# Performance work log

Measured on AMD Instinct MI355X. Metric: run time of the kernel, lower is better.

Reference implementation:

```python
import jax, jax.numpy as jnp
import numpy as np
from jax import lax

R, D, K = 8192, 1024, 1203          # proposals, feat dim, foreground classes
M = 128                             # per-class pre-NMS candidate budget (static)
TOPK = 300                          # test_topk_per_image
SCORE_THRESH = 1e-4
NMS_THRESH = 0.5
IMG_H, IMG_W = 800.0, 1333.0
NEG = -1e9
SCALE_CLAMP = float(np.log(1000.0 / 16.0))
BBOX_W = (10.0, 10.0, 5.0, 5.0)     # Box2BoxTransform weights


def setup_inputs() -> dict:
    key = jax.random.key(0)
    k0, k1, k2, k3 = jax.random.split(key, 4)
    feat = jax.random.normal(k0, (R, D), jnp.float32)
    u = jax.random.uniform(k1, (R, 4), jnp.float32)
    x1 = u[:, 0] * 1000.0
    y1 = u[:, 1] * 600.0
    bw = u[:, 2] * 300.0 + 16.0
    bh = u[:, 3] * 300.0 + 16.0
    proposals = jnp.stack([x1, y1, x1 + bw, y1 + bh], axis=1)  # [R,4] xyxy
    w_cls = jax.random.normal(k2, (D, K + 1), jnp.float32) * 0.02
    b_cls = jnp.zeros((K + 1,), jnp.float32)
    w_box = jax.random.normal(k3, (D, 4), jnp.float32) * 0.01
    b_box = jnp.zeros((4,), jnp.float32)
    return dict(feat=feat, proposals=proposals, w_cls=w_cls, b_cls=b_cls,
                w_box=w_box, b_box=b_box)


def _apply_deltas(deltas, boxes):
    # detectron2 Box2BoxTransform.apply_deltas, class-agnostic (R,4)
    wx, wy, ww, wh = BBOX_W
    widths = boxes[:, 2] - boxes[:, 0]
    heights = boxes[:, 3] - boxes[:, 1]
    ctr_x = boxes[:, 0] + 0.5 * widths
    ctr_y = boxes[:, 1] + 0.5 * heights
    dx = deltas[:, 0] / wx
    dy = deltas[:, 1] / wy
    dw = jnp.minimum(deltas[:, 2] / ww, SCALE_CLAMP)
    dh = jnp.minimum(deltas[:, 3] / wh, SCALE_CLAMP)
    pcx = dx * widths + ctr_x
    pcy = dy * heights + ctr_y
    pw = jnp.exp(dw) * widths
    ph = jnp.exp(dh) * heights
    return jnp.stack([pcx - 0.5 * pw, pcy - 0.5 * ph,
                      pcx + 0.5 * pw, pcy + 0.5 * ph], axis=1)


def _clip_boxes(b):
    x1 = jnp.clip(b[:, 0], 0.0, IMG_W)
    y1 = jnp.clip(b[:, 1], 0.0, IMG_H)
    x2 = jnp.clip(b[:, 2], 0.0, IMG_W)
    y2 = jnp.clip(b[:, 3], 0.0, IMG_H)
    return jnp.stack([x1, y1, x2, y2], axis=1)


def _iou_matrix(b):  # [M,4] -> [M,M]
    area = (b[:, 2] - b[:, 0]) * (b[:, 3] - b[:, 1])
    lt = jnp.maximum(b[:, None, :2], b[None, :, :2])
    rb = jnp.minimum(b[:, None, 2:], b[None, :, 2:])
    wh = jnp.clip(rb - lt, 0.0)
    inter = wh[..., 0] * wh[..., 1]
    return inter / (area[:, None] + area[None, :] - inter + 1e-6)


def _forward(feat, proposals, w_cls, b_cls, w_box, b_box):
    # dense heads
    logits = feat @ w_cls + b_cls                      # [R, K+1]
    probs = jax.nn.softmax(logits, axis=-1)
    scores = probs[:, :-1]                             # drop background -> [R, K]
    deltas = feat @ w_box + b_box                      # [R, 4] (class-agnostic)
    boxes = _clip_boxes(_apply_deltas(deltas, proposals))  # [R, 4]

    # score-threshold filter (masking instead of nonzero, jit-safe)
    masked = jnp.where(scores > SCORE_THRESH, scores, NEG)  # [R, K]

    def nms_one_class(cls_scores):  # [R] -> kept scores [M], proposal ids [M]
        vals, idx = lax.top_k(cls_scores, M)
        valid = vals > NEG * 0.5
        b = boxes[idx]                                 # [M, 4]
        iou = _iou_matrix(b)                           # [M, M]

        def body(keep, i):
            suppressed = jnp.any(keep & (iou[:, i] > NMS_THRESH))
            ki = valid[i] & jnp.logical_not(suppressed)
            return keep.at[i].set(ki), None

        keep, _ = lax.scan(body, jnp.zeros((M,), bool), jnp.arange(M))
        return jnp.where(keep, vals, NEG), idx

    per_scores, per_idx = jax.vmap(nms_one_class)(masked.T)  # [K, M] each

    # global top-k over surviving detections
    flat_scores = per_scores.reshape(-1)               # [K*M]
    top_vals, top_i = lax.top_k(flat_scores, TOPK)
    cls_ids = top_i // M                               # pred class per detection
    prop_ids = per_idx.reshape(-1)[top_i]              # original proposal index
    out_boxes = boxes[prop_ids]                        # [TOPK, 4]
    # pack: [x1,y1,x2,y2,score,class]
    return jnp.concatenate(
        [out_boxes, top_vals[:, None], cls_ids.astype(jnp.float32)[:, None]],
        axis=1)


def reference(feat, proposals, w_cls, b_cls, w_box, b_box):
    return _forward(feat, proposals, w_cls, b_cls, w_box, b_box)
```

## Files before the change

kernel.cpp:

```cpp
#include <hip/hip_runtime.h>
#include <math.h>
#include <stdint.h>

#define RR 8192
#define DD 1024
#define KCLS 1203
#define KP 1204
#define KP2 1216
#define NB 1280
#define MM 128
#define TOPKN 300
#define NFLAT (KCLS * MM)
#define NEGV (-1e9f)
#define SCLAMP 4.1351665567423563f

typedef __attribute__((ext_vector_type(8))) short bf16x8;
typedef __attribute__((ext_vector_type(4))) float f32x4;

__device__ __forceinline__ unsigned fmono(float f) {
  unsigned u = __float_as_uint(f);
  return (u & 0x80000000u) ? ~u : (u | 0x80000000u);
}
__device__ __forceinline__ float monof(unsigned u) {
  return __uint_as_float((u & 0x80000000u) ? (u ^ 0x80000000u) : ~u);
}
__device__ __forceinline__ float iou_f(float4 a, float4 b) {
  float areaA = (a.z - a.x) * (a.w - a.y);
  float areaB = (b.z - b.x) * (b.w - b.y);
  float lx = fmaxf(a.x, b.x), ly = fmaxf(a.y, b.y);
  float rx = fminf(a.z, b.z), ry = fminf(a.w, b.w);
  float w = fmaxf(rx - lx, 0.f), h = fmaxf(ry - ly, 0.f);
  float inter = w * h;
  return inter / (areaA + areaB - inter + 1e-6f);
}

__device__ __forceinline__ unsigned short bf16_rn(float x) {
  unsigned u = __float_as_uint(x);
  unsigned r = (u + 0x7FFFu + ((u >> 16) & 1u)) >> 16;
  return (unsigned short)r;
}
__device__ __forceinline__ float bf16f(unsigned short h) {
  return __uint_as_float(((unsigned)h) << 16);
}
__device__ __forceinline__ void split3(float x, unsigned short& h, unsigned short& m2, unsigned short& l) {
  h = bf16_rn(x);
  float r1 = x - bf16f(h);
  m2 = bf16_rn(r1);
  float r2 = r1 - bf16f(m2);
  l = bf16_rn(r2);
}

__global__ __launch_bounds__(256) void k_split_feat(const float* __restrict__ feat,
                                                    unsigned short* __restrict__ Ap) {
  const size_t i4 = (size_t)blockIdx.x * 256 + threadIdx.x;
  float4 v = *(const float4*)&feat[i4 * 4];
  ushort4 h, m2, l;
  split3(v.x, h.x, m2.x, l.x);
  split3(v.y, h.y, m2.y, l.y);
  split3(v.z, h.z, m2.z, l.z);
  split3(v.w, h.w, m2.w, l.w);
  const size_t P = (size_t)RR * DD;
  *(ushort4*)&Ap[0 * P + i4 * 4] = h;
  *(ushort4*)&Ap[1 * P + i4 * 4] = m2;
  *(ushort4*)&Ap[2 * P + i4 * 4] = l;
}

__global__ __launch_bounds__(256) void k_split_w(const float* __restrict__ wcls,
                                                 unsigned short* __restrict__ Btp) {
  __shared__ float st[64][65];
  const int c0 = blockIdx.x * 64, k0 = blockIdx.y * 64;
  const int tid = threadIdx.x;
  const int cc = tid & 63, kq = tid >> 6;
  for (int it = 0; it < 16; ++it) {
    int kl = it * 4 + kq;
    int c = c0 + cc;
    st[cc][kl] = (c < KP) ? wcls[(size_t)(k0 + kl) * KP + c] : 0.f;
  }
  __syncthreads();
  const int kk = tid & 63, cq = tid >> 6;
  const size_t P = (size_t)NB * DD;
  for (int it = 0; it < 16; ++it) {
    int cl = it * 4 + cq;
    float v = st[cl][kk];
    unsigned short h, m2, l;
    split3(v, h, m2, l);
    size_t off = (size_t)(c0 + cl) * DD + k0 + kk;
    Btp[0 * P + off] = h;
    Btp[1 * P + off] = m2;
    Btp[2 * P + off] = l;
  }
}

__global__ __launch_bounds__(512) void k_gemm_mfma(const unsigned short* __restrict__ Ap,
                                                   const unsigned short* __restrict__ Btp,
                                                   const float* __restrict__ bcls,
                                                   double* __restrict__ outlg) {
  __shared__ unsigned short As[3][128][40];
  __shared__ unsigned short Bs[3][128][40];
  const int tid = threadIdx.x;
  const int r0 = blockIdx.y * 128;
  const int c0 = blockIdx.x * 128;
  const int wid = tid >> 6, lane = tid & 63;
  const int wm = wid >> 2, wn = wid & 3;
  const int wrow = wm * 64, wcol = wn * 32;
  const int l15 = lane & 15, l4 = lane >> 4;

  f32x4 acc[4][2];
  double acc64[4][2][4];
#pragma unroll
  for (int mf = 0; mf < 4; ++mf)
#pragma unroll
    for (int nf = 0; nf < 2; ++nf) {
      acc[mf][nf] = (f32x4){0.f, 0.f, 0.f, 0.f};
#pragma unroll
      for (int q = 0; q < 4; ++q) acc64[mf][nf][q] = 0.0;
    }

  const size_t PA = (size_t)RR * DD;
  const size_t PB = (size_t)NB * DD;

  for (int kt = 0; kt < 32; ++kt) {
    __syncthreads();
#pragma unroll
    for (int it = 0; it < 3; ++it) {
      int c2 = it * 512 + tid;
      int plane = c2 >> 9;
      int rr2 = (c2 >> 2) & 127;
      int jc = (c2 & 3) << 3;
      const uint4 av = *(const uint4*)(Ap + (size_t)plane * PA + ((size_t)(r0 + rr2)) * DD + kt * 32 + jc);
      const uint4 bv = *(const uint4*)(Btp + (size_t)plane * PB + ((size_t)(c0 + rr2)) * DD + kt * 32 + jc);
      *(uint4*)&As[plane][rr2][jc] = av;
      *(uint4*)&Bs[plane][rr2][jc] = bv;
    }
    __syncthreads();

    bf16x8 bf[2][3];
#pragma unroll
    for (int nf = 0; nf < 2; ++nf)
#pragma unroll
      for (int p = 0; p < 3; ++p)
        bf[nf][p] = *(const bf16x8*)&Bs[p][wcol + nf * 16 + l15][l4 * 8];

#pragma unroll
    for (int mf = 0; mf < 4; ++mf) {
      bf16x8 a0 = *(const bf16x8*)&As[0][wrow + mf * 16 + l15][l4 * 8];
      bf16x8 a1 = *(const bf16x8*)&As[1][wrow + mf * 16 + l15][l4 * 8];
      bf16x8 a2 = *(const bf16x8*)&As[2][wrow + mf * 16 + l15][l4 * 8];
#pragma unroll
      for (int nf = 0; nf < 2; ++nf) {
        f32x4 a = acc[mf][nf];
        a = __builtin_amdgcn_mfma_f32_16x16x32_bf16(a0, bf[nf][0], a, 0, 0, 0);
        a = __builtin_amdgcn_mfma_f32_16x16x32_bf16(a0, bf[nf][1], a, 0, 0, 0);
        a = __builtin_amdgcn_mfma_f32_16x16x32_bf16(a1, bf[nf][0], a, 0, 0, 0);
        a = __builtin_amdgcn_mfma_f32_16x16x32_bf16(a0, bf[nf][2], a, 0, 0, 0);
        a = __builtin_amdgcn_mfma_f32_16x16x32_bf16(a2, bf[nf][0], a, 0, 0, 0);
        a = __builtin_amdgcn_mfma_f32_16x16x32_bf16(a1, bf[nf][1], a, 0, 0, 0);
        acc[mf][nf] = a;
      }
    }

    if (kt & 1) {
#pragma unroll
      for (int mf = 0; mf < 4; ++mf)
#pragma unroll
        for (int nf = 0; nf < 2; ++nf) {
#pragma unroll
          for (int q = 0; q < 4; ++q) acc64[mf][nf][q] += (double)acc[mf][nf][q];
          acc[mf][nf] = (f32x4){0.f, 0.f, 0.f, 0.f};
        }
    }
  }

#pragma unroll
  for (int mf = 0; mf < 4; ++mf)
#pragma unroll
    for (int nf = 0; nf < 2; ++nf) {
      int c = c0 + wcol + nf * 16 + l15;
      if (c < KP) {
#pragma unroll
        for (int q = 0; q < 4; ++q) {
          int r = r0 + wrow + mf * 16 + l4 * 4 + q;
          outlg[(size_t)r * KP2 + c] = acc64[mf][nf][q] + (double)bcls[c];
        }
      }
    }
}

__global__ __launch_bounds__(256) void k_softmax(const double* __restrict__ lg,
                                                 float* __restrict__ scoresA) {
  const int r = blockIdx.x;
  const int tid = threadIdx.x;
  __shared__ double ex[KP];
  __shared__ double red[256];
  double m = -1e300;
  for (int c = tid; c < KP; c += 256) {
    double z = lg[(size_t)r * KP2 + c];
    ex[c] = z;
    m = fmax(m, z);
  }
  red[tid] = m;
  __syncthreads();
  for (int off = 128; off; off >>= 1) {
    if (tid < off) red[tid] = fmax(red[tid], red[tid + off]);
    __syncthreads();
  }
  m = red[0];
  __syncthreads();
  double s = 0.0;
  for (int c = tid; c < KP; c += 256) {
    double e = exp(ex[c] - m);
    ex[c] = e;
    s += e;
  }
  red[tid] = s;
  __syncthreads();
  for (int off = 128; off; off >>= 1) {
    if (tid < off) red[tid] += red[tid + off];
    __syncthreads();
  }
  s = red[0];
  __syncthreads();
  for (int c = tid; c < KCLS; c += 256) {
    float f = (float)(ex[c] / s);
    scoresA[(size_t)r * KP2 + c] = (f > 1e-4f) ? f : NEGV;
  }
}

__global__ __launch_bounds__(256) void k_transposeS(const float* __restrict__ scoresA,
                                                    float* __restrict__ scoresT) {
  __shared__ float st[64][65];
  const int c0 = blockIdx.x * 64, r0 = blockIdx.y * 64;
  const int tid = threadIdx.x;
  const int cc = tid & 63, rq = tid >> 6;
  for (int it = 0; it < 16; ++it) {
    int r = r0 + it * 4 + rq;
    int c = c0 + cc;
    if (c < KCLS) st[cc][it * 4 + rq] = scoresA[(size_t)r * KP2 + c];
  }
  __syncthreads();
  const int rr = tid & 63, cq = tid >> 6;
  for (int it = 0; it < 16; ++it) {
    int c = c0 + it * 4 + cq;
    if (c < KCLS) scoresT[(size_t)c * RR + r0 + rr] = st[it * 4 + cq][rr];
  }
}

template <typename ZT>
__global__ __launch_bounds__(256) void k_gemm(const float* __restrict__ feat,
                                              const float* __restrict__ wcls,
                                              const float* __restrict__ bcls,
                                              ZT* __restrict__ out) {
  __shared__ float As[16][64];
  __shared__ float Bs[16][64];
  const int tid = threadIdx.x;
  const int c0 = blockIdx.x * 64;
  const int r0 = blockIdx.y * 64;
  const int tx4 = (tid & 15) << 2;
  const int ty4 = (tid >> 4) << 2;
  const int arow = tid >> 2, akq = (tid & 3) << 2;
  const int bk = tid >> 4, bcol = (tid & 15) << 2;

  float fa[4][4];
  double da[4][4];
#pragma unroll
  for (int i = 0; i < 4; i++)
#pragma unroll
    for (int j = 0; j < 4; j++) { fa[i][j] = 0.f; da[i][j] = 0.0; }

  for (int kt = 0; kt < DD / 16; ++kt) {
    float4 av = *(const float4*)&feat[(size_t)(r0 + arow) * DD + kt * 16 + akq];
    float4 bv;
    {
      int gc = c0 + bcol;
      const float* wrow = &wcls[(size_t)(kt * 16 + bk) * KP];
      if (gc + 3 < KP) {
        bv = *(const float4*)&wrow[gc];
      } else {
        bv.x = (gc + 0 < KP) ? wrow[gc + 0] : 0.f;
        bv.y = (gc + 1 < KP) ? wrow[gc + 1] : 0.f;
        bv.z = (gc + 2 < KP) ? wrow[gc + 2] : 0.f;
        bv.w = (gc + 3 < KP) ? wrow[gc + 3] : 0.f;
      }
    }
    __syncthreads();
    As[akq + 0][arow] = av.x;
    As[akq + 1][arow] = av.y;
    As[akq + 2][arow] = av.z;
    As[akq + 3][arow] = av.w;
    *(float4*)&Bs[bk][bcol] = bv;
    __syncthreads();
#pragma unroll
    for (int k = 0; k < 16; ++k) {
      float4 a = *(const float4*)&As[k][ty4];
      float4 b = *(const float4*)&Bs[k][tx4];
      float ax[4] = {a.x, a.y, a.z, a.w};
      float bx[4] = {b.x, b.y, b.z, b.w};
#pragma unroll
      for (int i = 0; i < 4; i++)
#pragma unroll
        for (int j = 0; j < 4; j++) fa[i][j] = fmaf(ax[i], bx[j], fa[i][j]);
    }
#pragma unroll
    for (int i = 0; i < 4; i++)
#pragma unroll
      for (int j = 0; j < 4; j++) { da[i][j] += (double)fa[i][j]; fa[i][j] = 0.f; }
  }
#pragma unroll
  for (int i = 0; i < 4; i++) {
    int r = r0 + ty4 + i;
#pragma unroll
    for (int j = 0; j < 4; j++) {
      int c = c0 + tx4 + j;
      if (c < KP) out[(size_t)r * KP + c] = (ZT)(da[i][j] + (double)bcls[c]);
    }
  }
}

template <typename ZT>
__global__ __launch_bounds__(256) void k_rowstats(const ZT* __restrict__ z,
                                                  double* __restrict__ rmax,
                                                  double* __restrict__ rsum) {
  const int r = blockIdx.x;
  const int tid = threadIdx.x;
  __shared__ double red[256];
  double m = -1e300;
  for (int c = tid; c < KP; c += 256) m = fmax(m, (double)z[(size_t)r * KP + c]);
  red[tid] = m;
  __syncthreads();
  for (int off = 128; off; off >>= 1) {
    if (tid < off) red[tid] = fmax(red[tid], red[tid + off]);
    __syncthreads();
  }
  m = red[0];
  __syncthreads();
  double s = 0.0;
  for (int c = tid; c < KP; c += 256) s += exp((double)z[(size_t)r * KP + c] - m);
  red[tid] = s;
  __syncthreads();
  for (int off = 128; off; off >>= 1) {
    if (tid < off) red[tid] += red[tid + off];
    __syncthreads();
  }
  if (tid == 0) { rmax[r] = m; rsum[r] = red[0]; }
}

template <typename ZT>
__global__ __launch_bounds__(256) void k_scores(const ZT* __restrict__ z,
                                                const double* __restrict__ rmax,
                                                const double* __restrict__ rsum,
                                                float* __restrict__ scoresT) {
  __shared__ float st[64][65];
  const int c0 = blockIdx.x * 64, r0 = blockIdx.y * 64;
  const int tid = threadIdx.x;
  const int cc = tid & 63, rq = tid >> 6;
  for (int it = 0; it < 16; ++it) {
    int r = r0 + it * 4 + rq;
    int c = c0 + cc;
    if (c < KCLS) {
      double zz = (double)z[(size_t)r * KP + c];
      double sc = exp(zz - rmax[r]) / rsum[r];
      float f = (float)sc;
      st[cc][it * 4 + rq] = (f > 1e-4f) ? f : NEGV;
    }
  }
  __syncthreads();
  const int rr = tid & 63, cq = tid >> 6;
  for (int it = 0; it < 16; ++it) {
    int c = c0 + it * 4 + cq;
    if (c < KCLS) scoresT[(size_t)c * RR + r0 + rr] = st[it * 4 + cq][rr];
  }
}

__global__ __launch_bounds__(256) void k_boxes(const float* __restrict__ feat,
                                               const float* __restrict__ wbox,
                                               const float* __restrict__ bbox,
                                               const float* __restrict__ props,
                                               float* __restrict__ boxes) {
  const int wid = threadIdx.x >> 6, lane = threadIdx.x & 63;
  const int r = blockIdx.x * 4 + wid;
  float p0 = 0, p1 = 0, p2 = 0, p3 = 0;
  for (int k = lane; k < DD; k += 64) {
    float f = feat[(size_t)r * DD + k];
    float4 w = *(const float4*)&wbox[k * 4];
    p0 = fmaf(f, w.x, p0);
    p1 = fmaf(f, w.y, p1);
    p2 = fmaf(f, w.z, p2);
    p3 = fmaf(f, w.w, p3);
  }
  for (int off = 32; off; off >>= 1) {
    p0 += __shfl_down(p0, off);
    p1 += __shfl_down(p1, off);
    p2 += __shfl_down(p2, off);
    p3 += __shfl_down(p3, off);
  }
  if (lane == 0) {
    p0 += bbox[0]; p1 += bbox[1]; p2 += bbox[2]; p3 += bbox[3];
    float4 pr = *(const float4*)&props[r * 4];
    float w = pr.z - pr.x, h = pr.w - pr.y;
    float cx = pr.x + 0.5f * w, cy = pr.y + 0.5f * h;
    float dx = p0 / 10.f, dy = p1 / 10.f;
    float dw = fminf(p2 / 5.f, SCLAMP), dh = fminf(p3 / 5.f, SCLAMP);
    float pcx = dx * w + cx, pcy = dy * h + cy;
    float pw = expf(dw) * w, ph = expf(dh) * h;
    float x1 = pcx - 0.5f * pw, y1 = pcy - 0.5f * ph;
    float x2 = pcx + 0.5f * pw, y2 = pcy + 0.5f * ph;
    x1 = fminf(fmaxf(x1, 0.f), 1333.f);
    x2 = fminf(fmaxf(x2, 0.f), 1333.f);
    y1 = fminf(fmaxf(y1, 0.f), 800.f);
    y2 = fminf(fmaxf(y2, 0.f), 800.f);
    *(float4*)&boxes[r * 4] = make_float4(x1, y1, x2, y2);
  }
}

template <bool DIRECT>
__global__ __launch_bounds__(256) void k_class(const float* __restrict__ scoresT,
                                               const float* __restrict__ lgf,
                                               const double* __restrict__ rmax,
                                               const double* __restrict__ rsum,
                                               const float* __restrict__ boxes,
                                               float* __restrict__ per_scores,
                                               int* __restrict__ per_idx,
                                               unsigned* __restrict__ hist1) {
  const int c = blockIdx.x, tid = threadIdx.x;
  __shared__ float sval[RR];
  __shared__ unsigned hist[256];
  __shared__ unsigned cum[256];
  __shared__ uint64_t skey[MM];
  __shared__ float4 sbox[MM];
  __shared__ int skeep[MM];
  __shared__ uint64_t s_prefix;
  __shared__ int s_need, s_cnt, s_supp;

  for (int r2 = tid; r2 < RR; r2 += 256) {
    float s;
    if (DIRECT) {
      double sc = exp((double)lgf[(size_t)r2 * KP + c] - rmax[r2]) / rsum[r2];
      float f = (float)sc;
      s = (f > 1e-4f) ? f : NEGV;
    } else {
      s = scoresT[(size_t)c * RR + r2];
    }
    sval[r2] = s;
  }
  if (tid == 0) { s_prefix = 0; s_need = MM; s_cnt = 0; }
  if (tid < MM) skey[tid] = 0;
  __syncthreads();

  for (int pass = 0; pass < 6; ++pass) {
    const int shift = 40 - 8 * pass;
    hist[tid] = 0;
    __syncthreads();
    uint64_t pre = s_prefix;
    int nd = s_need;
    for (int r2 = tid; r2 < RR; r2 += 256) {
      uint64_t key = ((uint64_t)fmono(sval[r2]) << 13) | (uint64_t)(8191 - r2);
      if ((key >> (shift + 8)) == (pre >> (shift + 8)))
        atomicAdd(&hist[(unsigned)(key >> shift) & 255u], 1u);
    }
    __syncthreads();
    cum[tid] = hist[tid];
    __syncthreads();
    for (int off = 1; off < 256; off <<= 1) {
      unsigned add = (tid + off < 256) ? cum[tid + off] : 0u;
      __syncthreads();
      cum[tid] += add;
      __syncthreads();
    }
    unsigned mycum = cum[tid];
    unsigned nxt = (tid < 255) ? cum[tid + 1] : 0u;
    if ((int)mycum >= nd && (int)nxt < nd) {
      s_prefix = pre | ((uint64_t)tid << shift);
      s_need = nd - (int)nxt;
    }
    __syncthreads();
  }
  const uint64_t kthr = s_prefix;
  for (int r2 = tid; r2 < RR; r2 += 256) {
    uint64_t key = ((uint64_t)fmono(sval[r2]) << 13) | (uint64_t)(8191 - r2);
    if (key >= kthr) {
      int p = atomicAdd(&s_cnt, 1);
      if (p < MM) skey[p] = key;
    }
  }
  __syncthreads();
  for (int kk2 = 2; kk2 <= MM; kk2 <<= 1)
    for (int j = kk2 >> 1; j > 0; j >>= 1) {
      __syncthreads();
      if (tid < MM) {
        int ixj = tid ^ j;
        if (ixj > tid) {
          uint64_t a = skey[tid], b = skey[ixj];
          bool desc = ((tid & kk2) == 0);
          if (desc ? (a < b) : (a > b)) { skey[tid] = b; skey[ixj] = a; }
        }
      }
    }
  __syncthreads();
  float myval = 0.f;
  int myidx = 0;
  bool valid = false;
  float4 mybox = make_float4(0, 0, 0, 0);
  if (tid < MM) {
    uint64_t key = skey[tid];
    myidx = 8191 - (int)(key & 0x1FFFu);
    myval = monof((unsigned)(key >> 13));
    valid = myval > -5e8f;
    mybox = *(const float4*)&boxes[myidx * 4];
    sbox[tid] = mybox;
    skeep[tid] = 0;
  }
  __syncthreads();
  for (int i = 0; i < MM; ++i) {
    if (tid == 0) s_supp = 0;
    __syncthreads();
    if (tid < i && skeep[tid]) {
      if (iou_f(mybox, sbox[i]) > 0.5f) s_supp = 1;
    }
    __syncthreads();
    if (tid == i) skeep[i] = (valid && !s_supp) ? 1 : 0;
  }
  __syncthreads();
  if (tid < MM) {
    per_scores[(size_t)c * MM + tid] = skeep[tid] ? myval : NEGV;
    per_idx[(size_t)c * MM + tid] = myidx;
    if (skeep[tid]) atomicAdd(&hist1[fmono(myval) >> 16], 1u);
  }
}

__global__ __launch_bounds__(1024) void k_sel1(const unsigned* __restrict__ hist, int* __restrict__ sel) {
  __shared__ unsigned red[1024];
  const int t = threadIdx.x;
  unsigned s = 0;
#pragma unroll 8
  for (int i = 0; i < 64; i++) s += hist[t * 64 + i];
  red[t] = s;
  __syncthreads();
  for (int off = 1; off < 1024; off <<= 1) {
    unsigned add = (t + off < 1024) ? red[t + off] : 0u;
    __syncthreads();
    red[t] += add;
    __syncthreads();
  }
  unsigned above = (t < 1023) ? red[t + 1] : 0u;
  if (red[t] >= (unsigned)TOPKN && above < (unsigned)TOPKN) {
    unsigned run = above;
    for (int b = 63; b >= 0; --b) {
      unsigned cb = hist[t * 64 + b];
      if (run < (unsigned)TOPKN && run + cb >= (unsigned)TOPKN) {
        sel[0] = t * 64 + b;
        sel[1] = (int)((unsigned)TOPKN - run);
      }
      run += cb;
    }
  }
}

__global__ __launch_bounds__(256) void k_hist2(const float* __restrict__ per_scores,
                                               const int* __restrict__ sel,
                                               unsigned* __restrict__ hist2) {
  const int f = blockIdx.x * 256 + threadIdx.x;
  if (f >= NFLAT) return;
  const unsigned p16 = (unsigned)sel[0];
  unsigned u = fmono(per_scores[f]);
  if ((u >> 16) == p16) atomicAdd(&hist2[u & 0xFFFFu], 1u);
}

__global__ __launch_bounds__(1024) void k_sel2(const unsigned* __restrict__ hist, int* __restrict__ sel) {
  __shared__ unsigned red[1024];
  __shared__ unsigned sneed, sp16;
  const int t = threadIdx.x;
  if (t == 0) { sneed = (unsigned)sel[1]; sp16 = (unsigned)sel[0]; }
  __syncthreads();
  const unsigned NEED = sneed;
  unsigned s = 0;
#pragma unroll 8
  for (int i = 0; i < 64; i++) s += hist[t * 64 + i];
  red[t] = s;
  __syncthreads();
  for (int off = 1; off < 1024; off <<= 1) {
    unsigned add = (t + off < 1024) ? red[t + off] : 0u;
    __syncthreads();
    red[t] += add;
    __syncthreads();
  }
  unsigned above = (t < 1023) ? red[t + 1] : 0u;
  if (red[t] >= NEED && above < NEED) {
    unsigned run = above;
    for (int b = 63; b >= 0; --b) {
      unsigned cb = hist[t * 64 + b];
      if (run < NEED && run + cb >= NEED) {
        sel[2] = (int)((sp16 << 16) | (unsigned)(t * 64 + b));
      }
      run += cb;
    }
  }
}

__global__ __launch_bounds__(256) void k_compact(const float* __restrict__ per_scores,
                                                 int* __restrict__ sel,
                                                 uint64_t* __restrict__ deflist,
                                                 uint64_t* __restrict__ tielist) {
  const int f = blockIdx.x * 256 + threadIdx.x;
  if (f >= NFLAT) return;
  const unsigned v32 = (unsigned)sel[2];
  unsigned u = fmono(per_scores[f]);
  if (u < v32) return;
  uint64_t key = ((uint64_t)u << 18) | (uint64_t)(262143 - f);
  if (u > v32) {
    int p = atomicAdd(&sel[4], 1);
    if (p < 512) deflist[p] = key;
  } else {
    int p = atomicAdd(&sel[5], 1);
    if (p < 512) tielist[p] = key;
  }
}

__global__ __launch_bounds__(1024) void k_final(const uint64_t* __restrict__ deflist,
                                                const uint64_t* __restrict__ tielist,
                                                const int* __restrict__ sel,
                                                const int* __restrict__ per_idx,
                                                const float* __restrict__ boxes,
                                                float* __restrict__ out) {
  __shared__ uint64_t skey[1024];
  const int t = threadIdx.x;
  const int n0 = min(sel[4], 512);
  const int n1 = min(sel[5], 512);
  uint64_t k = 0;
  if (t < n0) k = deflist[t];
  else if (t - n0 < n1) k = tielist[t - n0];
  skey[t] = k;
  __syncthreads();
  for (int kk2 = 2; kk2 <= 1024; kk2 <<= 1)
    for (int j = kk2 >> 1; j > 0; j >>= 1) {
      __syncthreads();
      int ixj = t ^ j;
      if (ixj > t) {
        uint64_t a = skey[t], b = skey[ixj];
        bool desc = ((t & kk2) == 0);
        if (desc ? (a < b) : (a > b)) { skey[t] = b; skey[ixj] = a; }
      }
    }
  __syncthreads();
  if (t < TOPKN) {
    uint64_t key = skey[t];
    int f = 262143 - (int)(key & 0x3FFFFu);
    float val = monof((unsigned)(key >> 18));
    int cls = f >> 7;
    int prop = per_idx[f];
    float4 b = *(const float4*)&boxes[prop * 4];
    float* o = &out[t * 6];
    o[0] = b.x; o[1] = b.y; o[2] = b.z; o[3] = b.w;
    o[4] = val; o[5] = (float)cls;
  }
}

extern "C" void kernel_launch(void* const* d_in, const int* in_sizes, int n_in,
                              void* d_out, int out_size, void* d_ws, size_t ws_size,
                              hipStream_t stream) {
  const float* feat = (const float*)d_in[0];
  const float* props = (const float*)d_in[1];
  const float* wcls = (const float*)d_in[2];
  const float* bcls = (const float*)d_in[3];
  const float* wbox = (const float*)d_in[4];
  const float* bbox = (const float*)d_in[5];
  float* out = (float*)d_out;
  char* ws = (char*)d_ws;

  size_t o = 0;
  auto al = [&](size_t b) { size_t cur = o; o += (b + 255) & ~(size_t)255; return cur; };
  const size_t o_boxes = al((size_t)RR * 4 * 4);
  const size_t o_ps = al((size_t)KCLS * MM * 4);
  const size_t o_pi = al((size_t)KCLS * MM * 4);
  const size_t o_rmax = al((size_t)RR * 8);
  const size_t o_rsum = al((size_t)RR * 8);
  const size_t o_hist1 = al((size_t)65536 * 4);
  const size_t o_hist2 = al((size_t)65536 * 4);
  const size_t o_sel = al((size_t)256);
  const size_t o_def = al((size_t)512 * 8);
  const size_t o_tie = al((size_t)512 * 8);
  const size_t fixed_end = o;

  float* boxes = (float*)(ws + o_boxes);
  float* per_scores = (float*)(ws + o_ps);
  int* per_idx = (int*)(ws + o_pi);
  double* rmax = (double*)(ws + o_rmax);
  double* rsum = (double*)(ws + o_rsum);
  unsigned* hist1 = (unsigned*)(ws + o_hist1);
  unsigned* hist2 = (unsigned*)(ws + o_hist2);
  int* sel = (int*)(ws + o_sel);
  uint64_t* deflist = (uint64_t*)(ws + o_def);
  uint64_t* tielist = (uint64_t*)(ws + o_tie);

  const size_t sz_A3 = ((size_t)3 * RR * DD * 2 + 255) & ~(size_t)255;
  const size_t sz_Bt = ((size_t)3 * NB * DD * 2 + 255) & ~(size_t)255;
  const size_t sz_lg2 = ((size_t)RR * KP2 * 8 + 255) & ~(size_t)255;
  const size_t needM = fixed_end + sz_A3 + sz_Bt + sz_lg2;

  const size_t sz_scT = ((size_t)KCLS * RR * 4 + 255) & ~(size_t)255;
  const size_t sz_lgD = ((size_t)RR * KP * 8 + 255) & ~(size_t)255;
  const size_t sz_lgF = ((size_t)RR * KP * 4 + 255) & ~(size_t)255;

  const bool pathM = ws_size >= needM;
  const bool pathA = !pathM && ws_size >= fixed_end + sz_scT + sz_lgD;
  const bool pathB = !pathM && !pathA && ws_size >= fixed_end + sz_scT + sz_lgF;

  const int gFlat = (NFLAT + 255) / 256;

  hipMemsetAsync(ws + o_hist1, 0, (o_sel - o_hist1) + 256, stream);

  k_boxes<<<RR / 4, 256, 0, stream>>>(feat, wbox, bbox, props, boxes);

  if (pathM) {
    unsigned short* Ap = (unsigned short*)(ws + fixed_end);
    unsigned short* Btp = (unsigned short*)(ws + fixed_end + sz_A3);
    double* lg = (double*)(ws + fixed_end + sz_A3 + sz_Bt);
    float* scoresA = (float*)(ws + fixed_end);
    float* scoresT = (float*)(ws + fixed_end + sz_A3 + sz_Bt);

    k_split_feat<<<(RR * DD / 4) / 256, 256, 0, stream>>>(feat, Ap);
    k_split_w<<<dim3(NB / 64, DD / 64), 256, 0, stream>>>(wcls, Btp);
    k_gemm_mfma<<<dim3(NB / 128, RR / 128), 512, 0, stream>>>(Ap, Btp, bcls, lg);
    k_softmax<<<RR, 256, 0, stream>>>(lg, scoresA);
    k_transposeS<<<dim3(KP2 / 64, RR / 64), 256, 0, stream>>>(scoresA, scoresT);
    k_class<false><<<KCLS, 256, 0, stream>>>(scoresT, nullptr, rmax, rsum, boxes, per_scores, per_idx, hist1);
  } else if (pathA) {
    float* scoresT = (float*)(ws + fixed_end);
    double* lg = (double*)(ws + fixed_end + sz_scT);
    k_gemm<double><<<dim3(19, 128), 256, 0, stream>>>(feat, wcls, bcls, lg);
    k_rowstats<double><<<RR, 256, 0, stream>>>(lg, rmax, rsum);
    k_scores<double><<<dim3(19, 128), 256, 0, stream>>>(lg, rmax, rsum, scoresT);
    k_class<false><<<KCLS, 256, 0, stream>>>(scoresT, nullptr, rmax, rsum, boxes, per_scores, per_idx, hist1);
  } else if (pathB) {
    float* scoresT = (float*)(ws + fixed_end);
    float* lg = (float*)(ws + fixed_end + sz_scT);
    k_gemm<float><<<dim3(19, 128), 256, 0, stream>>>(feat, wcls, bcls, lg);
    k_rowstats<float><<<RR, 256, 0, stream>>>(lg, rmax, rsum);
    k_scores<float><<<dim3(19, 128), 256, 0, stream>>>(lg, rmax, rsum, scoresT);
    k_class<false><<<KCLS, 256, 0, stream>>>(scoresT, nullptr, rmax, rsum, boxes, per_scores, per_idx, hist1);
  } else {
    float* lg = (float*)(ws + fixed_end);
    k_gemm<float><<<dim3(19, 128), 256, 0, stream>>>(feat, wcls, bcls, lg);
    k_rowstats<float><<<RR, 256, 0, stream>>>(lg, rmax, rsum);
    k_class<true><<<KCLS, 256, 0, stream>>>(nullptr, lg, rmax, rsum, boxes, per_scores, per_idx, hist1);
  }

  k_sel1<<<1, 1024, 0, stream>>>(hist1, sel);
  k_hist2<<<gFlat, 256, 0, stream>>>(per_scores, sel, hist2);
  k_sel2<<<1, 1024, 0, stream>>>(hist2, sel);
  k_compact<<<gFlat, 256, 0, stream>>>(per_scores, sel, deflist, tielist);
  k_final<<<1, 1024, 0, stream>>>(deflist, tielist, sel, per_idx, boxes, out);
}
```

Baseline: 710.8 us.

## Keep per-class scores in registers, use wave-shuffle scan and single-wave NMS

The per-class kernel now holds its 8192 scores as monotone keys in 32 registers per thread instead of a 32KB shared array, which lowers LDS use and should allow more blocks per CU. The 256-bin prefix scan, which used repeated block barriers, becomes a wavefront shuffle scan plus a small cross-wave total. The 128-step NMS loop now runs inside one 64-lane wave using shuffles and ballots, removing two block-wide barriers per step. The cost is higher register pressure from the 32-entry array, and the other three waves sit idle during NMS.

```diff
diff --git a/kernel.cpp b/kernel.cpp
--- a/kernel.cpp
+++ b/kernel.cpp
@@ -422,16 +422,17 @@
                                                int* __restrict__ per_idx,
                                                unsigned* __restrict__ hist1) {
   const int c = blockIdx.x, tid = threadIdx.x;
-  __shared__ float sval[RR];
+  const int lane = tid & 63, wid = tid >> 6;
   __shared__ unsigned hist[256];
-  __shared__ unsigned cum[256];
+  __shared__ unsigned wtot[4];
   __shared__ uint64_t skey[MM];
-  __shared__ float4 sbox[MM];
-  __shared__ int skeep[MM];
   __shared__ uint64_t s_prefix;
-  __shared__ int s_need, s_cnt, s_supp;
-
-  for (int r2 = tid; r2 < RR; r2 += 256) {
+  __shared__ int s_need, s_cnt;
+
+  unsigned u[32];
+#pragma unroll
+  for (int i = 0; i < 32; ++i) {
+    const int r2 = tid + (i << 8);
     float s;
     if (DIRECT) {
       double sc = exp((double)lgf[(size_t)r2 * KP + c] - rmax[r2]) / rsum[r2];
@@ -440,49 +441,53 @@
     } else {
       s = scoresT[(size_t)c * RR + r2];
     }
-    sval[r2] = s;
+    u[i] = fmono(s);
   }
   if (tid == 0) { s_prefix = 0; s_need = MM; s_cnt = 0; }
-  if (tid < MM) skey[tid] = 0;
   __syncthreads();
 
   for (int pass = 0; pass < 6; ++pass) {
     const int shift = 40 - 8 * pass;
     hist[tid] = 0;
     __syncthreads();
-    uint64_t pre = s_prefix;
-    int nd = s_need;
-    for (int r2 = tid; r2 < RR; r2 += 256) {
-      uint64_t key = ((uint64_t)fmono(sval[r2]) << 13) | (uint64_t)(8191 - r2);
+    const uint64_t pre = s_prefix;
+    const int nd = s_need;
+#pragma unroll
+    for (int i = 0; i < 32; ++i) {
+      uint64_t key = ((uint64_t)u[i] << 13) | (uint64_t)(8191 - (tid + (i << 8)));
       if ((key >> (shift + 8)) == (pre >> (shift + 8)))
         atomicAdd(&hist[(unsigned)(key >> shift) & 255u], 1u);
     }
     __syncthreads();
-    cum[tid] = hist[tid];
-    __syncthreads();
-    for (int off = 1; off < 256; off <<= 1) {
-      unsigned add = (tid + off < 256) ? cum[tid + off] : 0u;
-      __syncthreads();
-      cum[tid] += add;
-      __syncthreads();
-    }
-    unsigned mycum = cum[tid];
-    unsigned nxt = (tid < 255) ? cum[tid + 1] : 0u;
-    if ((int)mycum >= nd && (int)nxt < nd) {
+    const unsigned h = hist[tid];
+    unsigned x = h;
+#pragma unroll
+    for (int off = 1; off < 64; off <<= 1) {
+      unsigned y = __shfl_down(x, off);
+      x += (lane + off < 64) ? y : 0u;
+    }
+    if (lane == 0) wtot[wid] = x;
+    __syncthreads();
+    for (int w2 = wid + 1; w2 < 4; ++w2) x += wtot[w2];
+    const unsigned nxt = x - h;
+    if ((int)x >= nd && (int)nxt < nd) {
       s_prefix = pre | ((uint64_t)tid << shift);
       s_need = nd - (int)nxt;
     }
     __syncthreads();
   }
+
   const uint64_t kthr = s_prefix;
-  for (int r2 = tid; r2 < RR; r2 += 256) {
-    uint64_t key = ((uint64_t)fmono(sval[r2]) << 13) | (uint64_t)(8191 - r2);
+#pragma unroll
+  for (int i = 0; i < 32; ++i) {
+    uint64_t key = ((uint64_t)u[i] << 13) | (uint64_t)(8191 - (tid + (i << 8)));
     if (key >= kthr) {
       int p = atomicAdd(&s_cnt, 1);
       if (p < MM) skey[p] = key;
     }
   }
   __syncthreads();
+
   for (int kk2 = 2; kk2 <= MM; kk2 <<= 1)
     for (int j = kk2 >> 1; j > 0; j >>= 1) {
       __syncthreads();
@@ -496,34 +501,40 @@
       }
     }
   __syncthreads();
-  float myval = 0.f;
-  int myidx = 0;
-  bool valid = false;
-  float4 mybox = make_float4(0, 0, 0, 0);
-  if (tid < MM) {
-    uint64_t key = skey[tid];
-    myidx = 8191 - (int)(key & 0x1FFFu);
-    myval = monof((unsigned)(key >> 13));
-    valid = myval > -5e8f;
-    mybox = *(const float4*)&boxes[myidx * 4];
-    sbox[tid] = mybox;
-    skeep[tid] = 0;
-  }
-  __syncthreads();
-  for (int i = 0; i < MM; ++i) {
-    if (tid == 0) s_supp = 0;
-    __syncthreads();
-    if (tid < i && skeep[tid]) {
-      if (iou_f(mybox, sbox[i]) > 0.5f) s_supp = 1;
-    }
-    __syncthreads();
-    if (tid == i) skeep[i] = (valid && !s_supp) ? 1 : 0;
-  }
-  __syncthreads();
-  if (tid < MM) {
-    per_scores[(size_t)c * MM + tid] = skeep[tid] ? myval : NEGV;
-    per_idx[(size_t)c * MM + tid] = myidx;
-    if (skeep[tid]) atomicAdd(&hist1[fmono(myval) >> 16], 1u);
+
+  if (wid == 0) {
+    const uint64_t kA = skey[lane], kB = skey[lane + 64];
+    const int iA = 8191 - (int)(kA & 0x1FFFu);
+    const int iB = 8191 - (int)(kB & 0x1FFFu);
+    const float vA = monof((unsigned)(kA >> 13));
+    const float vB = monof((unsigned)(kB >> 13));
+    const bool validA = vA > -5e8f, validB = vB > -5e8f;
+    const float4 bA = *(const float4*)&boxes[iA * 4];
+    const float4 bB = *(const float4*)&boxes[iB * 4];
+    bool keepA = false, keepB = false;
+    for (int i = 0; i < MM; ++i) {
+      const int src = i & 63;
+      const bool hi = (i >= 64);
+      float cx = hi ? bB.x : bA.x, cy = hi ? bB.y : bA.y;
+      float cz = hi ? bB.z : bA.z, cw = hi ? bB.w : bA.w;
+      float4 bi;
+      bi.x = __shfl(cx, src);
+      bi.y = __shfl(cy, src);
+      bi.z = __shfl(cz, src);
+      bi.w = __shfl(cw, src);
+      const bool sA = keepA && (iou_f(bA, bi) > 0.5f);
+      const bool sB = keepB && (iou_f(bB, bi) > 0.5f);
+      const unsigned long long m = __ballot(sA) | __ballot(sB);
+      const bool supp = (m != 0ull);
+      if (!hi && lane == i) keepA = validA && !supp;
+      if (hi && lane == (i - 64)) keepB = validB && !supp;
+    }
+    per_scores[(size_t)c * MM + lane] = keepA ? vA : NEGV;
+    per_idx[(size_t)c * MM + lane] = iA;
+    per_scores[(size_t)c * MM + lane + 64] = keepB ? vB : NEGV;
+    per_idx[(size_t)c * MM + lane + 64] = iB;
+    if (keepA) atomicAdd(&hist1[fmono(vA) >> 16], 1u);
+    if (keepB) atomicAdd(&hist1[fmono(vB) >> 16], 1u);
   }
 }
 
```

Result: faster. 633.4 us (-10.9%).
